# Optimization experiments

Hardware: AMD Instinct MI355X
Metric: run time of the kernel (lower is better)

Reference implementation:

```python
import jax, jax.numpy as jnp
import numpy as np

N_EMBD = 1024
N_HEAD = 16
SEQ = 2048
BATCH = 2
NEG = -1000000000.0


def setup_inputs() -> dict:
    key = jax.random.key(0)
    k0, k1, k2 = jax.random.split(key, 3)
    return {
        "hidden_states": jax.random.normal(k0, (BATCH, SEQ, N_EMBD), dtype=jnp.float32),
        "w_attn": jax.random.normal(k1, (3 * N_EMBD, N_EMBD), dtype=jnp.float32) * 0.02,
        "b_attn": jnp.zeros((3 * N_EMBD,), dtype=jnp.float32),
        "w_proj": jax.random.normal(k2, (N_EMBD, N_EMBD), dtype=jnp.float32) * 0.02,
        "b_proj": jnp.zeros((N_EMBD,), dtype=jnp.float32),
    }


def reference(hidden_states, w_attn, b_attn, w_proj, b_proj):
    B, S, E = hidden_states.shape
    H = N_HEAD
    D = E // H
    # fused qkv projection (Conv1D: x @ kernel.T + bias)
    qkv = hidden_states @ w_attn.T + b_attn  # [B, S, 3E]
    q, k, v = jnp.split(qkv, 3, axis=-1)
    # split heads: [B, S, (H D)] -> [B, H, S, D]
    split = lambda t: t.reshape(B, S, H, D).transpose(0, 2, 1, 3)
    q, k, v = split(q), split(k), split(v)
    # scores [B, H, S, S]
    w = jnp.einsum("bhnd,bhmd->bhnm", q, k) * jax.lax.rsqrt(float(D))
    mask = jnp.tril(jnp.ones((S, S), dtype=jnp.float32))
    w = jnp.where(mask > 0, w, NEG)
    w = jax.nn.softmax(w, axis=-1)
    attn = jnp.einsum("bhnm,bhmd->bhnd", w, v)
    # merge heads -> [B, S, E]
    attn = attn.transpose(0, 2, 1, 3).reshape(B, S, E)
    return attn @ w_proj.T + b_proj
```

## Files before the change

kernel.cpp:

```cpp
#include <hip/hip_runtime.h>
#include <stdint.h>

#define S_LEN  2048
#define EMBD   1024
#define NHEAD  16
#define HDIM   64
#define BATCHN 2
#define ROWS   (BATCHN * S_LEN)

using bf16x8 = __attribute__((ext_vector_type(8))) __bf16;
using f32x4  = __attribute__((ext_vector_type(4))) float;
using f32x16 = __attribute__((ext_vector_type(16))) float;
using u32x4  = __attribute__((ext_vector_type(4))) unsigned;

typedef const __attribute__((address_space(1))) void* gas_ptr;
typedef __attribute__((address_space(3)))       void* las_ptr;

__device__ __forceinline__ void load_lds16(const void* g, void* l) {
    __builtin_amdgcn_global_load_lds((gas_ptr)(uintptr_t)g, (las_ptr)(uintptr_t)l, 16, 0, 0);
}

__device__ __forceinline__ unsigned short f2bf(float f) {
    unsigned u = __builtin_bit_cast(unsigned, f);
    u += 0x7fffu + ((u >> 16) & 1u);
    return (unsigned short)(u >> 16);
}

__device__ __forceinline__ unsigned pkbf(float a, float b) {
    unsigned r;
    asm("v_cvt_pk_bf16_f32 %0, %1, %2" : "=v"(r) : "v"(a), "v"(b));
    return r;
}

__device__ __forceinline__ int swz(int row, int ebase) {
    int byte = (row << 7) + (ebase << 1);
    byte ^= (row & 7) << 4;
    return byte >> 1;
}

__device__ __forceinline__ int swzV(int row, int ebase) {
    int byte = (row << 8) + (ebase << 1);
    byte ^= (row & 15) << 4;
    return byte >> 1;
}

__global__ void cvt3_f32_bf16(const float* __restrict__ s0,
                              const float* __restrict__ s1,
                              const float* __restrict__ s2,
                              unsigned short* __restrict__ d,
                              int n0, int n01, int ntot) {
    int i = blockIdx.x * blockDim.x + threadIdx.x;
    int stride = gridDim.x * blockDim.x;
    for (int idx = i * 4; idx < ntot; idx += stride * 4) {
        const float* s; int off;
        if (idx < n0)       { s = s0; off = idx; }
        else if (idx < n01) { s = s1; off = idx - n0; }
        else                { s = s2; off = idx - n01; }
        float4 f = *(const float4*)(s + off);
        uint2 p;
        p.x = (unsigned)f2bf(f.x) | ((unsigned)f2bf(f.y) << 16);
        p.y = (unsigned)f2bf(f.z) | ((unsigned)f2bf(f.w) << 16);
        *(uint2*)(d + idx) = p;
    }
}

#define SCALE_Q 0.18033688011112042f

__global__ __launch_bounds__(512, 2) void gemm_qkv(
    const unsigned short* __restrict__ A, const unsigned short* __restrict__ B,
    const float* __restrict__ bias,
    unsigned short* __restrict__ qb, unsigned short* __restrict__ kb,
    unsigned short* __restrict__ vb)
{
    __shared__ __align__(16) unsigned short sA[2][256 * 64];
    __shared__ __align__(16) unsigned short sB[2][192 * 64];

    const int tid  = threadIdx.x;
    const int wid  = tid >> 6;
    const int lane = tid & 63;
    const int g    = lane >> 4;
    const int c    = lane & 15;
    const int bm   = blockIdx.x * 256;
    const int bn   = blockIdx.y * 192;
    const int wm2  = (wid >> 2) * 128;
    const int wn2  = (wid & 3) * 48;
    const int K    = EMBD;
    const int NKT  = K / 64;

    f32x4 acc[8][3] = {};

    auto stage_a = [&](int kt, int buf) {
        const int k0 = kt * 64;
#pragma unroll
        for (int i = 0; i < 4; ++i) {
            int cbase = i * 512 + wid * 64;
            int cidx  = cbase + lane;
            int row   = cidx >> 3;
            int col   = ((cidx & 7) ^ (row & 7)) << 3;
            load_lds16(A + (size_t)(bm + row) * K + k0 + col, &sA[buf][cbase * 8]);
        }
    };
    auto stage_b = [&](int kt, int buf) {
        const int k0 = kt * 64;
#pragma unroll
        for (int i = 0; i < 3; ++i) {
            int cbase = i * 512 + wid * 64;
            int cidx  = cbase + lane;
            int row   = cidx >> 3;
            int col   = ((cidx & 7) ^ (row & 7)) << 3;
            load_lds16(B + (size_t)(bn + row) * K + k0 + col, &sB[buf][cbase * 8]);
        }
    };

    stage_a(0, 0);
    stage_b(0, 0);

    for (int kt = 0; kt < NKT; ++kt) {
        const int buf = kt & 1;
        asm volatile("s_waitcnt vmcnt(0)" ::: "memory");
        __builtin_amdgcn_s_barrier();

        bf16x8 bfr[3][2];
#pragma unroll
        for (int q = 0; q < 4; ++q) {
            if (kt + 1 < NKT) {
                if (q == 0) stage_a(kt + 1, buf ^ 1);
                if (q == 1) stage_b(kt + 1, buf ^ 1);
            }
            if (q == 0) {
#pragma unroll
                for (int j = 0; j < 3; ++j)
#pragma unroll
                    for (int kk = 0; kk < 2; ++kk)
                        bfr[j][kk] = *(const bf16x8*)
                            &sB[buf][swz(wn2 + j * 16 + c, kk * 32 + g * 8)];
            }
            bf16x8 af[2][2];
#pragma unroll
            for (int ii = 0; ii < 2; ++ii)
#pragma unroll
                for (int kk = 0; kk < 2; ++kk)
                    af[ii][kk] = *(const bf16x8*)
                        &sA[buf][swz(wm2 + (q * 2 + ii) * 16 + c, kk * 32 + g * 8)];

            __builtin_amdgcn_s_barrier();
            __builtin_amdgcn_s_setprio(1);
#pragma unroll
            for (int ii = 0; ii < 2; ++ii)
#pragma unroll
                for (int j = 0; j < 3; ++j)
#pragma unroll
                    for (int kk = 0; kk < 2; ++kk)
                        acc[q * 2 + ii][j] = __builtin_amdgcn_mfma_f32_16x16x32_bf16(
                            af[ii][kk], bfr[j][kk], acc[q * 2 + ii][j], 0, 0, 0);
            __builtin_amdgcn_s_setprio(0);
            __builtin_amdgcn_s_barrier();
        }
    }

    asm volatile("s_waitcnt vmcnt(0)" ::: "memory");

#pragma unroll
    for (int i = 0; i < 8; ++i)
#pragma unroll
        for (int j = 0; j < 3; ++j) {
            int n = bn + wn2 + j * 16 + c;
            float bv = bias[n];
            int which = n >> 10, h = (n & 1023) >> 6, d = n & 63;
            if (which < 2) {
                unsigned short* dst = (which == 0) ? qb : kb;
                float sc = (which == 0) ? SCALE_Q : 1.0f;
#pragma unroll
                for (int r = 0; r < 4; ++r) {
                    int m = bm + wm2 + i * 16 + g * 4 + r;
                    int b = m >> 11, s = m & 2047;
                    dst[(((size_t)b * NHEAD + h) * S_LEN + s) * HDIM + d] =
                        f2bf((acc[i][j][r] + bv) * sc);
                }
            } else {
                int m0 = bm + wm2 + i * 16 + g * 4;
                int b = m0 >> 11, s0 = m0 & 2047;
                uint2 p;
                p.x = pkbf(acc[i][j][0] + bv, acc[i][j][1] + bv);
                p.y = pkbf(acc[i][j][2] + bv, acc[i][j][3] + bv);
                *(uint2*)&vb[(((size_t)b * NHEAD + h) * HDIM + d) * S_LEN + s0] = p;
            }
        }
}

__global__ __launch_bounds__(256) void gemm_proj(
    const unsigned short* __restrict__ A, const unsigned short* __restrict__ B,
    const float* __restrict__ bias, float* __restrict__ Cout, int M, int N, int K)
{
    __shared__ __align__(16) unsigned short sA[128 * 64];
    __shared__ __align__(16) unsigned short sB[128 * 64];

    const int tid  = threadIdx.x;
    const int wid  = tid >> 6;
    const int lane = tid & 63;
    const int g    = lane >> 4;
    const int c    = lane & 15;
    const int bm   = blockIdx.x * 128;
    const int bn   = blockIdx.y * 128;
    const int wm   = (wid >> 1) * 64;
    const int wn   = (wid & 1) * 64;

    f32x4 acc[4][4] = {};

    for (int k0 = 0; k0 < K; k0 += 64) {
#pragma unroll
        for (int i = 0; i < 4; ++i) {
            int cidx = i * 256 + tid;
            int row  = cidx >> 3;
            int col  = ((cidx & 7) ^ (row & 7)) << 3;
            load_lds16(A + (size_t)(bm + row) * K + k0 + col,
                       &sA[i * 2048 + wid * 512]);
            load_lds16(B + (size_t)(bn + row) * K + k0 + col,
                       &sB[i * 2048 + wid * 512]);
        }
        __syncthreads();
#pragma unroll
        for (int kk = 0; kk < 2; ++kk) {
            bf16x8 af[4], bfr[4];
#pragma unroll
            for (int i = 0; i < 4; ++i)
                af[i] = *(const bf16x8*)&sA[swz(wm + i * 16 + c, kk * 32 + g * 8)];
#pragma unroll
            for (int j = 0; j < 4; ++j)
                bfr[j] = *(const bf16x8*)&sB[swz(wn + j * 16 + c, kk * 32 + g * 8)];
#pragma unroll
            for (int i = 0; i < 4; ++i)
#pragma unroll
                for (int j = 0; j < 4; ++j)
                    acc[i][j] = __builtin_amdgcn_mfma_f32_16x16x32_bf16(
                        af[i], bfr[j], acc[i][j], 0, 0, 0);
        }
        __syncthreads();
    }

#pragma unroll
    for (int i = 0; i < 4; ++i)
#pragma unroll
        for (int j = 0; j < 4; ++j) {
            int n = bn + wn + j * 16 + c;
            float bv = bias[n];
#pragma unroll
            for (int r = 0; r < 4; ++r) {
                int m = bm + wm + i * 16 + g * 4 + r;
                Cout[(size_t)m * N + n] = acc[i][j][r] + bv;
            }
        }
}

__global__ __launch_bounds__(512) void attn_kernel(
    const unsigned short* __restrict__ qbuf, const unsigned short* __restrict__ kbuf,
    const unsigned short* __restrict__ vtbuf, unsigned short* __restrict__ obuf)
{
    __shared__ __align__(16) unsigned short sK[3][128 * 64];
    __shared__ __align__(16) unsigned short sV[3][64 * 128];

    const int tid  = threadIdx.x;
    const int wid  = tid >> 6;
    const int wg   = wid & 3;
    const int grp  = wid >> 2;
    const int lane = tid & 63;
    const int hi   = lane >> 5;
    const int q5   = lane & 31;

    const int x  = blockIdx.x;
    const int j  = x >> 5;
    const int bh = x & 31;
    const int b  = bh >> 4, h = bh & 15;

    const int s  = grp ? j : (15 - j);
    const int TT = 16 - j;

    const unsigned short* Qh = qbuf  + (size_t)bh * S_LEN * HDIM;
    const unsigned short* Kh = kbuf  + (size_t)bh * S_LEN * HDIM;
    const unsigned short* Vt = vtbuf + (size_t)bh * HDIM * S_LEN;

    const int diag64 = 2 * s + (wg >> 1);
    const int qrow0  = 128 * s + 32 * wg;
    const int qg     = qrow0 + q5;

    auto stage = [&](int t, int buf) {
#pragma unroll
        for (int i = 0; i < 4; ++i) {
            int cbase = wg * 256 + i * 64;
            int cidx  = cbase + lane;
            if (grp == 0) {
                int row = cidx >> 3, col = ((cidx & 7) ^ (row & 7)) << 3;
                load_lds16(Kh + (size_t)(t * 128 + row) * HDIM + col,
                           &sK[buf][cbase * 8]);
            } else {
                int row = cidx >> 4, col = ((cidx & 15) ^ (row & 15)) << 3;
                load_lds16(Vt + (size_t)row * S_LEN + t * 128 + col,
                           &sV[buf][cbase * 8]);
            }
        }
    };

    bf16x8 aq[4];
#pragma unroll
    for (int ks = 0; ks < 4; ++ks)
        aq[ks] = *(const bf16x8*)&Qh[(size_t)qg * HDIM + ks * 16 + hi * 8];

    f32x16 o2[2] = {};
    float m_i = -1e30f, l_i = 0.f;

    stage(0, 0);
    stage(1, 1);

    for (int tt = 0; tt < TT; ++tt) {
        const int buf = tt % 3;
        asm volatile("s_waitcnt vmcnt(4)" ::: "memory");
        __builtin_amdgcn_s_barrier();
        stage(tt + 2 < TT ? tt + 2 : TT - 1, (tt + 2) % 3);

#pragma unroll
        for (int half = 0; half < 2; ++half) {
            const int t64 = 2 * tt + half;
            if (t64 > diag64) break;

            f32x16 acc[2] = {};
            __builtin_amdgcn_s_setprio(1);
#pragma unroll
            for (int ks = 0; ks < 4; ++ks) {
                bf16x8 k0 = *(const bf16x8*)&sK[buf][swz(half * 64 + q5,      ks * 16 + hi * 8)];
                bf16x8 k1 = *(const bf16x8*)&sK[buf][swz(half * 64 + q5 + 32, ks * 16 + hi * 8)];
                acc[0] = __builtin_amdgcn_mfma_f32_32x32x16_bf16(k0, aq[ks], acc[0], 0, 0, 0);
                acc[1] = __builtin_amdgcn_mfma_f32_32x32x16_bf16(k1, aq[ks], acc[1], 0, 0, 0);
            }
            __builtin_amdgcn_s_setprio(0);

            if (t64 == diag64) {
#pragma unroll
                for (int t2 = 0; t2 < 2; ++t2) {
                    int base = t64 * 64 + t2 * 32 + 4 * hi;
#pragma unroll
                    for (int r = 0; r < 16; ++r)
                        if (base + (r & 3) + 8 * (r >> 2) > qg) acc[t2][r] = -1e30f;
                }
            }

            float mx[8];
#pragma unroll
            for (int i = 0; i < 8; ++i)
                mx[i] = fmaxf(fmaxf(acc[i >> 2][(i & 3) * 4 + 0], acc[i >> 2][(i & 3) * 4 + 1]),
                              fmaxf(acc[i >> 2][(i & 3) * 4 + 2], acc[i >> 2][(i & 3) * 4 + 3]));
            float pm = fmaxf(fmaxf(fmaxf(mx[0], mx[1]), fmaxf(mx[2], mx[3])),
                             fmaxf(fmaxf(mx[4], mx[5]), fmaxf(mx[6], mx[7])));

            if (__any(pm > m_i + 8.0f)) {
                float pmr   = fmaxf(pm, __shfl_xor(pm, 32, 64));
                float m_new = fmaxf(m_i, pmr);
                float fac, dm = m_i - m_new;
                asm("v_exp_f32 %0, %1" : "=v"(fac) : "v"(dm));
                l_i *= fac;
                m_i  = m_new;
#pragma unroll
                for (int t2 = 0; t2 < 2; ++t2)
#pragma unroll
                    for (int r = 0; r < 16; ++r) o2[t2][r] *= fac;
            }

            unsigned pd[2][8];
            float lsum = 0.f;
#pragma unroll
            for (int t2 = 0; t2 < 2; ++t2) {
                float ev[16];
#pragma unroll
                for (int r = 0; r < 16; ++r) {
                    float a = acc[t2][r] - m_i;
                    asm("v_exp_f32 %0, %1" : "=v"(ev[r]) : "v"(a));
                }
                float s4[4];
#pragma unroll
                for (int u = 0; u < 4; ++u) {
                    s4[u] = (ev[4 * u] + ev[4 * u + 1]) + (ev[4 * u + 2] + ev[4 * u + 3]);
                    pd[t2][2 * u]     = pkbf(ev[4 * u],     ev[4 * u + 1]);
                    pd[t2][2 * u + 1] = pkbf(ev[4 * u + 2], ev[4 * u + 3]);
                }
                lsum += (s4[0] + s4[1]) + (s4[2] + s4[3]);
            }
            l_i += lsum;

            __builtin_amdgcn_s_setprio(1);
#pragma unroll
            for (int ks = 0; ks < 4; ++ks) {
                const int t2 = ks >> 1, k1 = ks & 1;
                unsigned p0 = pd[t2][4 * k1 + 0], p1 = pd[t2][4 * k1 + 1];
                unsigned p2 = pd[t2][4 * k1 + 2], p3 = pd[t2][4 * k1 + 3];
                asm("v_permlane32_swap_b32 %0, %1" : "+v"(p0), "+v"(p2));
                asm("v_permlane32_swap_b32 %0, %1" : "+v"(p1), "+v"(p3));
                u32x4 fw;
                fw[0] = p0; fw[1] = p1; fw[2] = p2; fw[3] = p3;
                bf16x8 pf = __builtin_bit_cast(bf16x8, fw);
                bf16x8 v0 = *(const bf16x8*)&sV[buf][swzV(q5,      half * 64 + ks * 16 + hi * 8)];
                bf16x8 v1 = *(const bf16x8*)&sV[buf][swzV(q5 + 32, half * 64 + ks * 16 + hi * 8)];
                o2[0] = __builtin_amdgcn_mfma_f32_32x32x16_bf16(v0, pf, o2[0], 0, 0, 0);
                o2[1] = __builtin_amdgcn_mfma_f32_32x32x16_bf16(v1, pf, o2[1], 0, 0, 0);
            }
            __builtin_amdgcn_s_setprio(0);
        }
    }

    asm volatile("s_waitcnt vmcnt(0)" ::: "memory");

    float l_full = l_i + __shfl_xor(l_i, 32, 64);
    float rl = 1.0f / l_full;
    unsigned short* orow = &obuf[((size_t)(b * S_LEN + qg)) * EMBD + h * HDIM];
#pragma unroll
    for (int t2 = 0; t2 < 2; ++t2)
#pragma unroll
        for (int u = 0; u < 4; ++u) {
            uint2 pw;
            pw.x = pkbf(o2[t2][4 * u] * rl,     o2[t2][4 * u + 1] * rl);
            pw.y = pkbf(o2[t2][4 * u + 2] * rl, o2[t2][4 * u + 3] * rl);
            *(uint2*)&orow[t2 * 32 + 4 * hi + 8 * u] = pw;
        }
}

extern "C" void kernel_launch(void* const* d_in, const int* in_sizes, int n_in,
                              void* d_out, int out_size, void* d_ws, size_t ws_size,
                              hipStream_t stream) {
    const float* hidden = (const float*)d_in[0];
    const float* w_attn = (const float*)d_in[1];
    const float* b_attn = (const float*)d_in[2];
    const float* w_proj = (const float*)d_in[3];
    const float* b_proj = (const float*)d_in[4];
    float* out = (float*)d_out;

    unsigned short* Xbf  = (unsigned short*)d_ws;
    unsigned short* Wabf = Xbf  + (size_t)ROWS * EMBD;
    unsigned short* Wpbf = Wabf + (size_t)3 * EMBD * EMBD;
    unsigned short* qb   = Wpbf + (size_t)EMBD * EMBD;
    unsigned short* kb   = qb + (size_t)BATCHN * NHEAD * S_LEN * HDIM;
    unsigned short* vtb  = kb + (size_t)BATCHN * NHEAD * S_LEN * HDIM;
    unsigned short* ob   = vtb + (size_t)BATCHN * NHEAD * S_LEN * HDIM;

    const int n0   = ROWS * EMBD;
    const int n01  = n0 + 3 * EMBD * EMBD;
    const int ntot = n01 + EMBD * EMBD;
    cvt3_f32_bf16<<<2048, 256, 0, stream>>>(hidden, w_attn, w_proj, Xbf,
                                            n0, n01, ntot);

    gemm_qkv<<<dim3(ROWS / 256, 3 * EMBD / 192), 512, 0, stream>>>(
        Xbf, Wabf, b_attn, qb, kb, vtb);

    attn_kernel<<<dim3(256), 512, 0, stream>>>(qb, kb, vtb, ob);

    gemm_proj<<<dim3(ROWS / 128, EMBD / 128), 256, 0, stream>>>(
        ob, Wpbf, b_proj, out, ROWS, EMBD, EMBD);
}
```

Baseline: 102.5 us.

## Balance causal attention work by letting the short-row group steal heavy-row tiles

Each block pairs a long causal query tile (group 0) with a short one (group 1). Group 1 now also processes the later KV tiles of the long row with its own online-softmax state. The two partial results are then merged through LDS using log-sum-exp rescaling. This evens out per-wave work inside a block so the long group no longer sets the block's duration, at the cost of extra registers (a second Q fragment and accumulator), an LDS merge step and additional barriers.

```diff
diff --git a/kernel.cpp b/kernel.cpp
--- a/kernel.cpp
+++ b/kernel.cpp
@@ -268,20 +268,23 @@
     const int q5   = lane & 31;
 
     const int x  = blockIdx.x;
-    const int j  = x >> 5;
+    const int jj = x >> 5;
     const int bh = x & 31;
     const int b  = bh >> 4, h = bh & 15;
 
-    const int s  = grp ? j : (15 - j);
-    const int TT = 16 - j;
+    const int sH   = 15 - jj;
+    const int sOwn = grp ? jj : sH;
+    const int TT   = 16 - jj;
 
     const unsigned short* Qh = qbuf  + (size_t)bh * S_LEN * HDIM;
     const unsigned short* Kh = kbuf  + (size_t)bh * S_LEN * HDIM;
     const unsigned short* Vt = vtbuf + (size_t)bh * HDIM * S_LEN;
 
-    const int diag64 = 2 * s + (wg >> 1);
-    const int qrow0  = 128 * s + 32 * wg;
-    const int qg     = qrow0 + q5;
+    const int diagOwn = 2 * sOwn + (wg >> 1);
+    const int diagA   = 2 * sH + (wg >> 1);
+    const int csplit  = 16 + (wg >> 1);
+    const int qgOwn   = 128 * sOwn + 32 * wg + q5;
+    const int qgSt    = 128 * sH + 32 * wg + q5;
 
     auto stage = [&](int t, int buf) {
 #pragma unroll
@@ -300,13 +303,101 @@
         }
     };
 
-    bf16x8 aq[4];
+    bf16x8 aq[4], aqS[4];
 #pragma unroll
     for (int ks = 0; ks < 4; ++ks)
-        aq[ks] = *(const bf16x8*)&Qh[(size_t)qg * HDIM + ks * 16 + hi * 8];
-
-    f32x16 o2[2] = {};
+        aq[ks] = *(const bf16x8*)&Qh[(size_t)qgOwn * HDIM + ks * 16 + hi * 8];
+    if (grp == 1) {
+#pragma unroll
+        for (int ks = 0; ks < 4; ++ks)
+            aqS[ks] = *(const bf16x8*)&Qh[(size_t)qgSt * HDIM + ks * 16 + hi * 8];
+    }
+
+    f32x16 o2[2] = {}, oS[2] = {};
     float m_i = -1e30f, l_i = 0.f;
+    float mS  = -1e30f, lS  = 0.f;
+
+    auto tile64 = [&](int t64, int buf, int half, const bf16x8* aqv, int qgv,
+                      int diagv, float& m, float& l, f32x16& oA, f32x16& oB) {
+        f32x16 acc[2] = {};
+        __builtin_amdgcn_s_setprio(1);
+#pragma unroll
+        for (int ks = 0; ks < 4; ++ks) {
+            bf16x8 k0 = *(const bf16x8*)&sK[buf][swz(half * 64 + q5,      ks * 16 + hi * 8)];
+            bf16x8 k1 = *(const bf16x8*)&sK[buf][swz(half * 64 + q5 + 32, ks * 16 + hi * 8)];
+            acc[0] = __builtin_amdgcn_mfma_f32_32x32x16_bf16(k0, aqv[ks], acc[0], 0, 0, 0);
+            acc[1] = __builtin_amdgcn_mfma_f32_32x32x16_bf16(k1, aqv[ks], acc[1], 0, 0, 0);
+        }
+        __builtin_amdgcn_s_setprio(0);
+
+        if (t64 == diagv) {
+#pragma unroll
+            for (int t2 = 0; t2 < 2; ++t2) {
+                int base = t64 * 64 + t2 * 32 + 4 * hi;
+#pragma unroll
+                for (int r = 0; r < 16; ++r)
+                    if (base + (r & 3) + 8 * (r >> 2) > qgv) acc[t2][r] = -1e30f;
+            }
+        }
+
+        float mx[8];
+#pragma unroll
+        for (int i = 0; i < 8; ++i)
+            mx[i] = fmaxf(fmaxf(acc[i >> 2][(i & 3) * 4 + 0], acc[i >> 2][(i & 3) * 4 + 1]),
+                          fmaxf(acc[i >> 2][(i & 3) * 4 + 2], acc[i >> 2][(i & 3) * 4 + 3]));
+        float pm = fmaxf(fmaxf(fmaxf(mx[0], mx[1]), fmaxf(mx[2], mx[3])),
+                         fmaxf(fmaxf(mx[4], mx[5]), fmaxf(mx[6], mx[7])));
+
+        if (__any(pm > m + 8.0f)) {
+            float pmr   = fmaxf(pm, __shfl_xor(pm, 32, 64));
+            float m_new = fmaxf(m, pmr);
+            float fac, dm = m - m_new;
+            asm("v_exp_f32 %0, %1" : "=v"(fac) : "v"(dm));
+            l *= fac;
+            m  = m_new;
+#pragma unroll
+            for (int r = 0; r < 16; ++r) { oA[r] *= fac; oB[r] *= fac; }
+        }
+
+        unsigned pd[2][8];
+        float lsum = 0.f;
+#pragma unroll
+        for (int t2 = 0; t2 < 2; ++t2) {
+            float ev[16];
+#pragma unroll
+            for (int r = 0; r < 16; ++r) {
+                float a = acc[t2][r] - m;
+                asm("v_exp_f32 %0, %1" : "=v"(ev[r]) : "v"(a));
+            }
+            float s4[4];
+#pragma unroll
+            for (int u = 0; u < 4; ++u) {
+                s4[u] = (ev[4 * u] + ev[4 * u + 1]) + (ev[4 * u + 2] + ev[4 * u + 3]);
+                pd[t2][2 * u]     = pkbf(ev[4 * u],     ev[4 * u + 1]);
+                pd[t2][2 * u + 1] = pkbf(ev[4 * u + 2], ev[4 * u + 3]);
+            }
+            lsum += (s4[0] + s4[1]) + (s4[2] + s4[3]);
+        }
+        l += lsum;
+
+        __builtin_amdgcn_s_setprio(1);
+#pragma unroll
+        for (int ks = 0; ks < 4; ++ks) {
+            const int t2 = ks >> 1, k1 = ks & 1;
+            unsigned p0 = pd[t2][4 * k1 + 0], p1 = pd[t2][4 * k1 + 1];
+            unsigned p2 = pd[t2][4 * k1 + 2], p3 = pd[t2][4 * k1 + 3];
+            asm("v_permlane32_swap_b32 %0, %1" : "+v"(p0), "+v"(p2));
+            asm("v_permlane32_swap_b32 %0, %1" : "+v"(p1), "+v"(p3));
+            u32x4 fw;
+            fw[0] = p0; fw[1] = p1; fw[2] = p2; fw[3] = p3;
+            bf16x8 pf = __builtin_bit_cast(bf16x8, fw);
+            bf16x8 v0 = *(const bf16x8*)&sV[buf][swzV(q5,      half * 64 + ks * 16 + hi * 8)];
+            bf16x8 v1 = *(const bf16x8*)&sV[buf][swzV(q5 + 32, half * 64 + ks * 16 + hi * 8)];
+            oA = __builtin_amdgcn_mfma_f32_32x32x16_bf16(v0, pf, oA, 0, 0, 0);
+            oB = __builtin_amdgcn_mfma_f32_32x32x16_bf16(v1, pf, oB, 0, 0, 0);
+        }
+        __builtin_amdgcn_s_setprio(0);
+    };
 
     stage(0, 0);
     stage(1, 1);
@@ -320,96 +411,51 @@
 #pragma unroll
         for (int half = 0; half < 2; ++half) {
             const int t64 = 2 * tt + half;
-            if (t64 > diag64) break;
-
-            f32x16 acc[2] = {};
-            __builtin_amdgcn_s_setprio(1);
-#pragma unroll
-            for (int ks = 0; ks < 4; ++ks) {
-                bf16x8 k0 = *(const bf16x8*)&sK[buf][swz(half * 64 + q5,      ks * 16 + hi * 8)];
-                bf16x8 k1 = *(const bf16x8*)&sK[buf][swz(half * 64 + q5 + 32, ks * 16 + hi * 8)];
-                acc[0] = __builtin_amdgcn_mfma_f32_32x32x16_bf16(k0, aq[ks], acc[0], 0, 0, 0);
-                acc[1] = __builtin_amdgcn_mfma_f32_32x32x16_bf16(k1, aq[ks], acc[1], 0, 0, 0);
-            }
-            __builtin_amdgcn_s_setprio(0);
-
-            if (t64 == diag64) {
-#pragma unroll
-                for (int t2 = 0; t2 < 2; ++t2) {
-                    int base = t64 * 64 + t2 * 32 + 4 * hi;
-#pragma unroll
-                    for (int r = 0; r < 16; ++r)
-                        if (base + (r & 3) + 8 * (r >> 2) > qg) acc[t2][r] = -1e30f;
-                }
-            }
-
-            float mx[8];
-#pragma unroll
-            for (int i = 0; i < 8; ++i)
-                mx[i] = fmaxf(fmaxf(acc[i >> 2][(i & 3) * 4 + 0], acc[i >> 2][(i & 3) * 4 + 1]),
-                              fmaxf(acc[i >> 2][(i & 3) * 4 + 2], acc[i >> 2][(i & 3) * 4 + 3]));
-            float pm = fmaxf(fmaxf(fmaxf(mx[0], mx[1]), fmaxf(mx[2], mx[3])),
-                             fmaxf(fmaxf(mx[4], mx[5]), fmaxf(mx[6], mx[7])));
-
-            if (__any(pm > m_i + 8.0f)) {
-                float pmr   = fmaxf(pm, __shfl_xor(pm, 32, 64));
-                float m_new = fmaxf(m_i, pmr);
-                float fac, dm = m_i - m_new;
-                asm("v_exp_f32 %0, %1" : "=v"(fac) : "v"(dm));
-                l_i *= fac;
-                m_i  = m_new;
-#pragma unroll
-                for (int t2 = 0; t2 < 2; ++t2)
-#pragma unroll
-                    for (int r = 0; r < 16; ++r) o2[t2][r] *= fac;
-            }
-
-            unsigned pd[2][8];
-            float lsum = 0.f;
-#pragma unroll
-            for (int t2 = 0; t2 < 2; ++t2) {
-                float ev[16];
-#pragma unroll
-                for (int r = 0; r < 16; ++r) {
-                    float a = acc[t2][r] - m_i;
-                    asm("v_exp_f32 %0, %1" : "=v"(ev[r]) : "v"(a));
-                }
-                float s4[4];
-#pragma unroll
-                for (int u = 0; u < 4; ++u) {
-                    s4[u] = (ev[4 * u] + ev[4 * u + 1]) + (ev[4 * u + 2] + ev[4 * u + 3]);
-                    pd[t2][2 * u]     = pkbf(ev[4 * u],     ev[4 * u + 1]);
-                    pd[t2][2 * u + 1] = pkbf(ev[4 * u + 2], ev[4 * u + 3]);
-                }
-                lsum += (s4[0] + s4[1]) + (s4[2] + s4[3]);
-            }
-            l_i += lsum;
-
-            __builtin_amdgcn_s_setprio(1);
-#pragma unroll
-            for (int ks = 0; ks < 4; ++ks) {
-                const int t2 = ks >> 1, k1 = ks & 1;
-                unsigned p0 = pd[t2][4 * k1 + 0], p1 = pd[t2][4 * k1 + 1];
-                unsigned p2 = pd[t2][4 * k1 + 2], p3 = pd[t2][4 * k1 + 3];
-                asm("v_permlane32_swap_b32 %0, %1" : "+v"(p0), "+v"(p2));
-                asm("v_permlane32_swap_b32 %0, %1" : "+v"(p1), "+v"(p3));
-                u32x4 fw;
-                fw[0] = p0; fw[1] = p1; fw[2] = p2; fw[3] = p3;
-                bf16x8 pf = __builtin_bit_cast(bf16x8, fw);
-                bf16x8 v0 = *(const bf16x8*)&sV[buf][swzV(q5,      half * 64 + ks * 16 + hi * 8)];
-                bf16x8 v1 = *(const bf16x8*)&sV[buf][swzV(q5 + 32, half * 64 + ks * 16 + hi * 8)];
-                o2[0] = __builtin_amdgcn_mfma_f32_32x32x16_bf16(v0, pf, o2[0], 0, 0, 0);
-                o2[1] = __builtin_amdgcn_mfma_f32_32x32x16_bf16(v1, pf, o2[1], 0, 0, 0);
-            }
-            __builtin_amdgcn_s_setprio(0);
+            if (grp == 0) {
+                if (t64 < csplit)
+                    tile64(t64, buf, half, aq, qgOwn, -1, m_i, l_i, o2[0], o2[1]);
+            } else {
+                if (t64 <= diagOwn)
+                    tile64(t64, buf, half, aq, qgOwn, diagOwn, m_i, l_i, o2[0], o2[1]);
+                else if (t64 >= csplit && t64 <= diagA)
+                    tile64(t64, buf, half, aqS, qgSt, diagA, mS, lS, oS[0], oS[1]);
+            }
         }
     }
 
     asm volatile("s_waitcnt vmcnt(0)" ::: "memory");
+    __builtin_amdgcn_s_barrier();
+
+    float* mrg = (float*)&sK[0][0];
+    if (grp == 1) {
+        int base = (wg * 64 + lane) * 34;
+#pragma unroll
+        for (int t2 = 0; t2 < 2; ++t2)
+#pragma unroll
+            for (int r = 0; r < 16; ++r) mrg[base + t2 * 16 + r] = oS[t2][r];
+        mrg[base + 32] = mS;
+        mrg[base + 33] = lS;
+    }
+    __builtin_amdgcn_s_barrier();
+
+    if (grp == 0) {
+        int base = (wg * 64 + lane) * 34;
+        float mB = mrg[base + 32], lB = mrg[base + 33];
+        float mN = fmaxf(m_i, mB);
+        float fA, fB, dA = m_i - mN, dB = mB - mN;
+        asm("v_exp_f32 %0, %1" : "=v"(fA) : "v"(dA));
+        asm("v_exp_f32 %0, %1" : "=v"(fB) : "v"(dB));
+        l_i = l_i * fA + lB * fB;
+#pragma unroll
+        for (int t2 = 0; t2 < 2; ++t2)
+#pragma unroll
+            for (int r = 0; r < 16; ++r)
+                o2[t2][r] = o2[t2][r] * fA + mrg[base + t2 * 16 + r] * fB;
+    }
 
     float l_full = l_i + __shfl_xor(l_i, 32, 64);
     float rl = 1.0f / l_full;
-    unsigned short* orow = &obuf[((size_t)(b * S_LEN + qg)) * EMBD + h * HDIM];
+    unsigned short* orow = &obuf[((size_t)(b * S_LEN + qgOwn)) * EMBD + h * HDIM];
 #pragma unroll
     for (int t2 = 0; t2 < 2; ++t2)
 #pragma unroll
```

Result: slower. 108.7 us (+6.0%).
